# Kernel tuning notes

Measured on AMD Instinct MI355X. Metric: run time of the kernel, lower is better.

Reference implementation:

```python
import jax, jax.numpy as jnp
import numpy as np


def setup_inputs() -> dict:
    key = jax.random.key(0)
    k1, k2 = jax.random.split(key)
    x = jax.random.normal(k1, (8, 256, 16, 32, 32), dtype=jnp.float32)
    mem = jax.random.normal(k2, (200, 256), dtype=jnp.float32)
    return {"x": x, "mem": mem}


def reference(x, mem):
    B, C, T, H, W = x.shape
    # (B, N, C) tokens where N = T*H*W
    x_flat = x.reshape(B, C, -1).transpose(0, 2, 1)
    # scores against memory slots: (B, N, mem_dim)
    att = jax.nn.softmax(jnp.einsum('bnc,mc->bnm', x_flat, mem), axis=-1)
    # read from memory: (B, N, C)
    mem_out = jnp.einsum('bnm,mc->bnc', att, mem)
    return mem_out.transpose(0, 2, 1).reshape(B, C, T, H, W)
```

## Files before the change

kernel.cpp:

```cpp
#include <hip/hip_runtime.h>

typedef _Float16 h16x8 __attribute__((ext_vector_type(8)));
typedef float f32x4 __attribute__((ext_vector_type(4)));

#define MFMA16F(a, b, c) __builtin_amdgcn_mfma_f32_16x16x32_f16((a), (b), (c), 0, 0, 0)

#define GLOAD16(gp, lp)                                                        \
  __builtin_amdgcn_global_load_lds(                                            \
      (const __attribute__((address_space(1))) unsigned int*)(gp),             \
      (__attribute__((address_space(3))) unsigned int*)(lp), 16, 0, 0)

#define FENCE() __builtin_amdgcn_sched_barrier(0)


__global__ __launch_bounds__(256) void prep_mem(const float* __restrict__ mem,
                                                unsigned short* __restrict__ M16,
                                                unsigned short* __restrict__ MB) {
  const int s = blockIdx.x;
  const int c = threadIdx.x;
  const float v = (s < 200) ? mem[s * 256 + c] : 0.0f;
  const _Float16 hv = (_Float16)v;
  const unsigned short hb = __builtin_bit_cast(unsigned short, hv);
  M16[s * 256 + c] = hb;
  if (s < 224) {
    const int kk = s >> 5;
    const int th = (s >> 4) & 1;
    const int hh = (s >> 2) & 3;
    const int rr = s & 3;
    const int j = th * 4 + rr;
    MB[kk * 8192 + (c >> 4) * 512 + hh * 128 + (c & 15) * 8 + j] = hb;
  }
}

__global__ __launch_bounds__(1024, 4) void fused_mem_attn(
    const float* __restrict__ x, const unsigned short* __restrict__ M16,
    const unsigned short* __restrict__ MB, float* __restrict__ out) {
  __shared__ alignas(128) char lds[131072];

  const int tid = threadIdx.x;
  const int wave = tid >> 6;
  const int lane = tid & 63;
  const int t16 = lane & 15;
  const int h = lane >> 4;

  const int Lb = tid ^ ((tid >> 3) & 7);
  const int srcOff = (Lb >> 2) * 512 + (Lb & 3) * 16;
  const int q16 = ((((t16 << 2) + h) ^ (t16 >> 1)) << 4);

  const long gtok0 = (long)blockIdx.x * 256;
  const int b = (int)(gtok0 >> 14);
  const int bn0 = (int)(gtok0 & 16383);
  const float* xb = x + ((long)b << 22) + bn0 + (wave * 16 + t16);
  float* outT = out + ((long)b << 22) + bn0 + (wave * 16 + 4 * h) + ((long)t16 << 14);

  const char* M16B = (const char*)M16;
  const char* MBB = (const char*)MB;

#define XLOAD(ks)                                                              \
  _Pragma("unroll") for (int j = 0; j < 8; ++j) {                              \
    xr[(ks) % 3][j] = xb[(long)((ks) * 32 + h * 8 + j) << 14];                 \
  }

  float xr[3][8];
  f32x4 acc[14] = {};

#define COMPUTE(ks)                                                            \
  {                                                                            \
    if ((ks) < 6) XLOAD((ks) + 2);                                             \
    h16x8 xh, xl;                                                              \
    _Pragma("unroll") for (int j = 0; j < 8; ++j) {                            \
      const float f = xr[(ks) % 3][j];                                         \
      const _Float16 hi_ = (_Float16)f;                                        \
      xh[j] = hi_;                                                             \
      xl[j] = (_Float16)(f - (float)hi_);                                      \
    }                                                                          \
    const char* sb = lds + (ks) * 16384;                                       \
    __builtin_amdgcn_s_setprio(1);                                             \
    _Pragma("unroll") for (int tt = 0; tt < 13; ++tt) {                        \
      const h16x8 ah = *(const h16x8*)(sb + tt * 1024 + q16);                  \
      acc[tt] = MFMA16F(ah, xh, acc[tt]);                                      \
      acc[tt] = MFMA16F(ah, xl, acc[tt]);                                      \
    }                                                                          \
    __builtin_amdgcn_s_setprio(0);                                             \
    FENCE();                                                                   \
  }

  XLOAD(0);
  XLOAD(1);
#pragma unroll
  for (int ks = 0; ks < 8; ++ks)
    GLOAD16(M16B + srcOff + ks * 64, lds + ks * 16384 + tid * 16);
  __syncthreads();

  COMPUTE(0) COMPUTE(1) COMPUTE(2) COMPUTE(3)
  COMPUTE(4) COMPUTE(5) COMPUTE(6) COMPUTE(7)

  __syncthreads();

#pragma unroll
  for (int k = 0; k < 7; ++k)
    GLOAD16(MBB + k * 16384 + tid * 16, lds + k * 16384 + tid * 16);

  float m = -3.0e38f;
#pragma unroll
  for (int tt = 0; tt < 12; ++tt)
#pragma unroll
    for (int r = 0; r < 4; ++r) m = fmaxf(m, acc[tt][r]);
#pragma unroll
  for (int r = 0; r < 4; ++r)
    if (192 + h * 4 + r < 200) m = fmaxf(m, acc[12][r]);
  m = fmaxf(m, __shfl_xor(m, 16, 64));
  m = fmaxf(m, __shfl_xor(m, 32, 64));
  float s = 0.f;
#pragma unroll
  for (int tt = 0; tt < 12; ++tt)
#pragma unroll
    for (int r = 0; r < 4; ++r) {
      const float p = __expf(acc[tt][r] - m);
      acc[tt][r] = p;
      s += p;
    }
#pragma unroll
  for (int r = 0; r < 4; ++r) {
    const bool ok = (192 + h * 4 + r) < 200;
    const float p = ok ? __expf(acc[12][r] - m) : 0.f;
    acc[12][r] = p;
    s += p;
  }
  s += __shfl_xor(s, 16, 64);
  s += __shfl_xor(s, 32, 64);
  const float inv = 1.f / s;

  h16x8 pa[7];
#pragma unroll
  for (int kk = 0; kk < 7; ++kk)
#pragma unroll
    for (int j = 0; j < 8; ++j)
      pa[kk][j] = (_Float16)(inv * acc[2 * kk + (j >> 2)][j & 3]);

  __syncthreads();

#pragma unroll
  for (int ct = 0; ct < 16; ++ct) {
    f32x4 a2 = {0.f, 0.f, 0.f, 0.f};
    __builtin_amdgcn_s_setprio(1);
#pragma unroll
    for (int kk = 0; kk < 7; ++kk) {
      const h16x8 bt = *(const h16x8*)(lds + kk * 16384 + ct * 1024 + lane * 16);
      a2 = MFMA16F(pa[kk], bt, a2);
    }
    __builtin_amdgcn_s_setprio(0);
    *(f32x4*)(outT + ((long)ct << 18)) = a2;
  }
#undef XLOAD
#undef COMPUTE
}

extern "C" void kernel_launch(void* const* d_in, const int* in_sizes, int n_in,
                              void* d_out, int out_size, void* d_ws, size_t ws_size,
                              hipStream_t stream) {
  const float* x = (const float*)d_in[0];
  const float* mem = (const float*)d_in[1];
  float* out = (float*)d_out;

  unsigned short* M16 = (unsigned short*)d_ws;
  unsigned short* MB = M16 + 256 * 256;

  prep_mem<<<dim3(256), dim3(256), 0, stream>>>(mem, M16, MB);
  fused_mem_attn<<<dim3(512), dim3(1024), 0, stream>>>(x, M16, MB, out);
}
```

Baseline: 68.50 us.

## Process two token tiles per wave and shrink blocks to 768 threads

Each wave now handles 32 tokens (two 16-token groups), so every LDS-loaded memory fragment feeds two MFMAs instead of one, halving LDS reads per unit of compute. Blocks shrink to 12 waves (384 tokens) with a 342-block grid and a validity guard for the tail wave, and the shared memory staging is split across threads so all LDS slots are still filled. The setprio hints are removed, the last-slot pa fragment is zero-padded, and register pressure roughly doubles for accumulators, which risks lower occupancy or spills.

```diff
diff --git a/kernel.cpp b/kernel.cpp
--- a/kernel.cpp
+++ b/kernel.cpp
@@ -32,7 +32,7 @@
   }
 }
 
-__global__ __launch_bounds__(1024, 4) void fused_mem_attn(
+__global__ __launch_bounds__(768, 3) void fused_mem_attn(
     const float* __restrict__ x, const unsigned short* __restrict__ M16,
     const unsigned short* __restrict__ MB, float* __restrict__ out) {
   __shared__ alignas(128) char lds[131072];
@@ -43,53 +43,73 @@
   const int t16 = lane & 15;
   const int h = lane >> 4;
 
-  const int Lb = tid ^ ((tid >> 3) & 7);
-  const int srcOff = (Lb >> 2) * 512 + (Lb & 3) * 16;
+  const int P0 = tid;
+  const int L0 = P0 ^ ((P0 >> 3) & 7);
+  const int srcOff0 = (L0 >> 2) * 512 + (L0 & 3) * 16;
+  const int P1 = 768 + tid;
+  const int L1 = P1 ^ ((P1 >> 3) & 7);
+  const int srcOff1 = (L1 >> 2) * 512 + (L1 & 3) * 16;
+  const bool own1 = (tid < 256);
+
   const int q16 = ((((t16 << 2) + h) ^ (t16 >> 1)) << 4);
 
-  const long gtok0 = (long)blockIdx.x * 256;
-  const int b = (int)(gtok0 >> 14);
-  const int bn0 = (int)(gtok0 & 16383);
-  const float* xb = x + ((long)b << 22) + bn0 + (wave * 16 + t16);
-  float* outT = out + ((long)b << 22) + bn0 + (wave * 16 + 4 * h) + ((long)t16 << 14);
+  const long tw_raw = (long)blockIdx.x * 384 + wave * 32;
+  const bool wvalid = (tw_raw + 31) < 131072;
+  const long tw = wvalid ? tw_raw : 0;
+
+  const long T0 = tw + t16;
+  const long T1 = tw + 16 + t16;
+  const float* xb0 = x + ((T0 >> 14) << 22) + (T0 & 16383);
+  const float* xb1 = x + ((T1 >> 14) << 22) + (T1 & 16383);
+  const long S0 = tw + 4 * h;
+  const long S1 = tw + 16 + 4 * h;
+  float* ob0 = out + ((S0 >> 14) << 22) + (S0 & 16383) + ((long)t16 << 14);
+  float* ob1 = out + ((S1 >> 14) << 22) + (S1 & 16383) + ((long)t16 << 14);
 
   const char* M16B = (const char*)M16;
   const char* MBB = (const char*)MB;
 
 #define XLOAD(ks)                                                              \
   _Pragma("unroll") for (int j = 0; j < 8; ++j) {                              \
-    xr[(ks) % 3][j] = xb[(long)((ks) * 32 + h * 8 + j) << 14];                 \
-  }
-
-  float xr[3][8];
-  f32x4 acc[14] = {};
+    const long o_ = (long)((ks) * 32 + h * 8 + j) << 14;                       \
+    xr[(ks) & 1][0][j] = xb0[o_];                                              \
+    xr[(ks) & 1][1][j] = xb1[o_];                                              \
+  }
+
+  float xr[2][2][8];
+  f32x4 acc[13][2] = {};
 
 #define COMPUTE(ks)                                                            \
   {                                                                            \
-    if ((ks) < 6) XLOAD((ks) + 2);                                             \
-    h16x8 xh, xl;                                                              \
+    if ((ks) < 7) XLOAD((ks) + 1);                                             \
+    h16x8 xh0, xl0, xh1, xl1;                                                  \
     _Pragma("unroll") for (int j = 0; j < 8; ++j) {                            \
-      const float f = xr[(ks) % 3][j];                                         \
-      const _Float16 hi_ = (_Float16)f;                                        \
-      xh[j] = hi_;                                                             \
-      xl[j] = (_Float16)(f - (float)hi_);                                      \
+      const float f0 = xr[(ks) & 1][0][j];                                     \
+      const float f1 = xr[(ks) & 1][1][j];                                     \
+      const _Float16 h0_ = (_Float16)f0;                                       \
+      const _Float16 h1_ = (_Float16)f1;                                       \
+      xh0[j] = h0_;                                                            \
+      xl0[j] = (_Float16)(f0 - (float)h0_);                                    \
+      xh1[j] = h1_;                                                            \
+      xl1[j] = (_Float16)(f1 - (float)h1_);                                    \
     }                                                                          \
     const char* sb = lds + (ks) * 16384;                                       \
-    __builtin_amdgcn_s_setprio(1);                                             \
     _Pragma("unroll") for (int tt = 0; tt < 13; ++tt) {                        \
       const h16x8 ah = *(const h16x8*)(sb + tt * 1024 + q16);                  \
-      acc[tt] = MFMA16F(ah, xh, acc[tt]);                                      \
-      acc[tt] = MFMA16F(ah, xl, acc[tt]);                                      \
+      acc[tt][0] = MFMA16F(ah, xh0, acc[tt][0]);                               \
+      acc[tt][1] = MFMA16F(ah, xh1, acc[tt][1]);                               \
+      acc[tt][0] = MFMA16F(ah, xl0, acc[tt][0]);                               \
+      acc[tt][1] = MFMA16F(ah, xl1, acc[tt][1]);                               \
     }                                                                          \
-    __builtin_amdgcn_s_setprio(0);                                             \
     FENCE();                                                                   \
   }
 
   XLOAD(0);
-  XLOAD(1);
-#pragma unroll
-  for (int ks = 0; ks < 8; ++ks)
-    GLOAD16(M16B + srcOff + ks * 64, lds + ks * 16384 + tid * 16);
+#pragma unroll
+  for (int ks = 0; ks < 8; ++ks) {
+    GLOAD16(M16B + srcOff0 + ks * 64, lds + ks * 16384 + P0 * 16);
+    if (own1) GLOAD16(M16B + srcOff1 + ks * 64, lds + ks * 16384 + P1 * 16);
+  }
   __syncthreads();
 
   COMPUTE(0) COMPUTE(1) COMPUTE(2) COMPUTE(3)
@@ -98,59 +118,78 @@
   __syncthreads();
 
 #pragma unroll
-  for (int k = 0; k < 7; ++k)
-    GLOAD16(MBB + k * 16384 + tid * 16, lds + k * 16384 + tid * 16);
-
-  float m = -3.0e38f;
-#pragma unroll
-  for (int tt = 0; tt < 12; ++tt)
-#pragma unroll
-    for (int r = 0; r < 4; ++r) m = fmaxf(m, acc[tt][r]);
-#pragma unroll
-  for (int r = 0; r < 4; ++r)
-    if (192 + h * 4 + r < 200) m = fmaxf(m, acc[12][r]);
-  m = fmaxf(m, __shfl_xor(m, 16, 64));
-  m = fmaxf(m, __shfl_xor(m, 32, 64));
-  float s = 0.f;
-#pragma unroll
-  for (int tt = 0; tt < 12; ++tt)
+  for (int k = 0; k < 7; ++k) {
+    GLOAD16(MBB + k * 16384 + P0 * 16, lds + k * 16384 + P0 * 16);
+    if (own1) GLOAD16(MBB + k * 16384 + P1 * 16, lds + k * 16384 + P1 * 16);
+  }
+  FENCE();
+
+  float inv[2];
+#pragma unroll
+  for (int g = 0; g < 2; ++g) {
+    float m = -3.0e38f;
+#pragma unroll
+    for (int tt = 0; tt < 12; ++tt)
+#pragma unroll
+      for (int r = 0; r < 4; ++r) m = fmaxf(m, acc[tt][g][r]);
+#pragma unroll
+    for (int r = 0; r < 4; ++r)
+      if (192 + h * 4 + r < 200) m = fmaxf(m, acc[12][g][r]);
+    m = fmaxf(m, __shfl_xor(m, 16, 64));
+    m = fmaxf(m, __shfl_xor(m, 32, 64));
+    float s = 0.f;
+#pragma unroll
+    for (int tt = 0; tt < 12; ++tt)
+#pragma unroll
+      for (int r = 0; r < 4; ++r) {
+        const float p = __expf(acc[tt][g][r] - m);
+        acc[tt][g][r] = p;
+        s += p;
+      }
 #pragma unroll
     for (int r = 0; r < 4; ++r) {
-      const float p = __expf(acc[tt][r] - m);
-      acc[tt][r] = p;
+      const bool ok = (192 + h * 4 + r) < 200;
+      const float p = ok ? __expf(acc[12][g][r] - m) : 0.f;
+      acc[12][g][r] = p;
       s += p;
     }
-#pragma unroll
-  for (int r = 0; r < 4; ++r) {
-    const bool ok = (192 + h * 4 + r) < 200;
-    const float p = ok ? __expf(acc[12][r] - m) : 0.f;
-    acc[12][r] = p;
-    s += p;
-  }
-  s += __shfl_xor(s, 16, 64);
-  s += __shfl_xor(s, 32, 64);
-  const float inv = 1.f / s;
-
-  h16x8 pa[7];
-#pragma unroll
-  for (int kk = 0; kk < 7; ++kk)
+    s += __shfl_xor(s, 16, 64);
+    s += __shfl_xor(s, 32, 64);
+    inv[g] = 1.f / s;
+  }
+
+  h16x8 pa[7][2];
+#pragma unroll
+  for (int kk = 0; kk < 6; ++kk)
+#pragma unroll
+    for (int g = 0; g < 2; ++g)
+#pragma unroll
+      for (int j = 0; j < 8; ++j)
+        pa[kk][g][j] = (_Float16)(inv[g] * acc[2 * kk + (j >> 2)][g][j & 3]);
+#pragma unroll
+  for (int g = 0; g < 2; ++g)
 #pragma unroll
     for (int j = 0; j < 8; ++j)
-      pa[kk][j] = (_Float16)(inv * acc[2 * kk + (j >> 2)][j & 3]);
+      pa[6][g][j] = (j < 4) ? (_Float16)(inv[g] * acc[12][g][j & 3])
+                            : (_Float16)0.f;
 
   __syncthreads();
 
 #pragma unroll
   for (int ct = 0; ct < 16; ++ct) {
-    f32x4 a2 = {0.f, 0.f, 0.f, 0.f};
-    __builtin_amdgcn_s_setprio(1);
+    f32x4 a0 = {0.f, 0.f, 0.f, 0.f};
+    f32x4 a1 = {0.f, 0.f, 0.f, 0.f};
 #pragma unroll
     for (int kk = 0; kk < 7; ++kk) {
       const h16x8 bt = *(const h16x8*)(lds + kk * 16384 + ct * 1024 + lane * 16);
-      a2 = MFMA16F(pa[kk], bt, a2);
+      a0 = MFMA16F(pa[kk][0], bt, a0);
+      a1 = MFMA16F(pa[kk][1], bt, a1);
     }
-    __builtin_amdgcn_s_setprio(0);
-    *(f32x4*)(outT + ((long)ct << 18)) = a2;
+    if (wvalid) {
+      *(f32x4*)(ob0 + ((long)ct << 18)) = a0;
+      *(f32x4*)(ob1 + ((long)ct << 18)) = a1;
+    }
+    FENCE();
   }
 #undef XLOAD
 #undef COMPUTE
@@ -167,5 +206,5 @@
   unsigned short* MB = M16 + 256 * 256;
 
   prep_mem<<<dim3(256), dim3(256), 0, stream>>>(mem, M16, MB);
-  fused_mem_attn<<<dim3(512), dim3(1024), 0, stream>>>(x, M16, MB, out);
+  fused_mem_attn<<<dim3(342), dim3(768), 0, stream>>>(x, M16, MB, out);
 }
```

After: 84.40 us. 23.2% more time.

## Process two token tiles per block, prefetching second tile's x during first softmax

Applied to the files above, without the earlier changes.

Each block now handles 512 tokens in two sequential 256-token passes, and the grid is halved to 256 blocks. The x loads for the second tile are issued during the first tile's softmax so their latency overlaps compute. The M16 and MB tables are still re-staged into LDS for every pass, so LDS traffic is unchanged. The aim is to hide global-load latency and cut block launch overhead, at the cost of fewer blocks than the 256 CUs can use well (each block already uses 128KB of LDS) and a longer serial chain per block.

```diff
diff --git a/kernel.cpp b/kernel.cpp
--- a/kernel.cpp
+++ b/kernel.cpp
@@ -47,26 +47,35 @@
   const int srcOff = (Lb >> 2) * 512 + (Lb & 3) * 16;
   const int q16 = ((((t16 << 2) + h) ^ (t16 >> 1)) << 4);
 
-  const long gtok0 = (long)blockIdx.x * 256;
-  const int b = (int)(gtok0 >> 14);
-  const int bn0 = (int)(gtok0 & 16383);
-  const float* xb = x + ((long)b << 22) + bn0 + (wave * 16 + t16);
-  float* outT = out + ((long)b << 22) + bn0 + (wave * 16 + 4 * h) + ((long)t16 << 14);
+  const long base0 = (long)blockIdx.x * 512;
+  const int b = (int)(base0 >> 14);
+  const int bn0 = (int)(base0 & 16383);
+  const float* xA = x + ((long)b << 22) + bn0 + (wave * 16 + t16);
+  const float* xBp = xA + 256;
+  float* oA = out + ((long)b << 22) + bn0 + (wave * 16 + 4 * h) + ((long)t16 << 14);
+  float* oB = oA + 256;
 
   const char* M16B = (const char*)M16;
   const char* MBB = (const char*)MB;
 
-#define XLOAD(ks)                                                              \
+  float xr[3][8];
+
+#define STAGE_M16()                                                            \
+  _Pragma("unroll") for (int ks = 0; ks < 8; ++ks)                             \
+      GLOAD16(M16B + srcOff + ks * 64, lds + ks * 16384 + tid * 16);
+
+#define STAGE_MB()                                                             \
+  _Pragma("unroll") for (int k = 0; k < 7; ++k)                                \
+      GLOAD16(MBB + k * 16384 + tid * 16, lds + k * 16384 + tid * 16);
+
+#define XLOAD(XP, ks)                                                          \
   _Pragma("unroll") for (int j = 0; j < 8; ++j) {                              \
-    xr[(ks) % 3][j] = xb[(long)((ks) * 32 + h * 8 + j) << 14];                 \
-  }
-
-  float xr[3][8];
-  f32x4 acc[14] = {};
-
-#define COMPUTE(ks)                                                            \
+    xr[(ks) % 3][j] = (XP)[(long)((ks) * 32 + h * 8 + j) << 14];               \
+  }
+
+#define COMPUTE(XP, ks)                                                        \
   {                                                                            \
-    if ((ks) < 6) XLOAD((ks) + 2);                                             \
+    if ((ks) < 6) XLOAD(XP, (ks) + 2);                                         \
     h16x8 xh, xl;                                                              \
     _Pragma("unroll") for (int j = 0; j < 8; ++j) {                            \
       const float f = xr[(ks) % 3][j];                                         \
@@ -85,75 +94,101 @@
     FENCE();                                                                   \
   }
 
-  XLOAD(0);
-  XLOAD(1);
-#pragma unroll
-  for (int ks = 0; ks < 8; ++ks)
-    GLOAD16(M16B + srcOff + ks * 64, lds + ks * 16384 + tid * 16);
+#define SOFTMAX_REPACK()                                                       \
+  {                                                                            \
+    float m = -3.0e38f;                                                        \
+    _Pragma("unroll") for (int tt = 0; tt < 12; ++tt)                          \
+        _Pragma("unroll") for (int r = 0; r < 4; ++r)                          \
+            m = fmaxf(m, acc[tt][r]);                                          \
+    _Pragma("unroll") for (int r = 0; r < 4; ++r)                              \
+        if (192 + h * 4 + r < 200) m = fmaxf(m, acc[12][r]);                   \
+    m = fmaxf(m, __shfl_xor(m, 16, 64));                                       \
+    m = fmaxf(m, __shfl_xor(m, 32, 64));                                       \
+    float s = 0.f;                                                             \
+    _Pragma("unroll") for (int tt = 0; tt < 12; ++tt)                          \
+        _Pragma("unroll") for (int r = 0; r < 4; ++r) {                        \
+      const float p = __expf(acc[tt][r] - m);                                  \
+      acc[tt][r] = p;                                                          \
+      s += p;                                                                  \
+    }                                                                          \
+    _Pragma("unroll") for (int r = 0; r < 4; ++r) {                            \
+      const bool ok = (192 + h * 4 + r) < 200;                                 \
+      const float p = ok ? __expf(acc[12][r] - m) : 0.f;                       \
+      acc[12][r] = p;                                                          \
+      s += p;                                                                  \
+    }                                                                          \
+    s += __shfl_xor(s, 16, 64);                                                \
+    s += __shfl_xor(s, 32, 64);                                                \
+    const float inv = 1.f / s;                                                 \
+    _Pragma("unroll") for (int kk = 0; kk < 7; ++kk)                           \
+        _Pragma("unroll") for (int j = 0; j < 8; ++j)                          \
+            pa[kk][j] = (_Float16)(inv * acc[2 * kk + (j >> 2)][j & 3]);       \
+  }
+
+#define PV_PHASE(OB)                                                           \
+  _Pragma("unroll") for (int ct = 0; ct < 16; ++ct) {                          \
+    f32x4 a2 = {0.f, 0.f, 0.f, 0.f};                                           \
+    __builtin_amdgcn_s_setprio(1);                                             \
+    _Pragma("unroll") for (int kk = 0; kk < 7; ++kk) {                         \
+      const h16x8 bt =                                                         \
+          *(const h16x8*)(lds + kk * 16384 + ct * 1024 + lane * 16);           \
+      a2 = MFMA16F(pa[kk], bt, a2);                                            \
+    }                                                                          \
+    __builtin_amdgcn_s_setprio(0);                                             \
+    *(f32x4*)((OB) + ((long)ct << 18)) = a2;                                   \
+  }
+
+  {
+    XLOAD(xA, 0);
+    XLOAD(xA, 1);
+    STAGE_M16();
+    __syncthreads();
+
+    f32x4 acc[14] = {};
+    h16x8 pa[7];
+
+    COMPUTE(xA, 0) COMPUTE(xA, 1) COMPUTE(xA, 2) COMPUTE(xA, 3)
+    COMPUTE(xA, 4) COMPUTE(xA, 5) COMPUTE(xA, 6) COMPUTE(xA, 7)
+
+    __syncthreads();
+    STAGE_MB();
+    XLOAD(xBp, 0);
+    XLOAD(xBp, 1);
+
+    SOFTMAX_REPACK();
+
+    __syncthreads();
+
+    PV_PHASE(oA);
+  }
+
   __syncthreads();
 
-  COMPUTE(0) COMPUTE(1) COMPUTE(2) COMPUTE(3)
-  COMPUTE(4) COMPUTE(5) COMPUTE(6) COMPUTE(7)
-
-  __syncthreads();
-
-#pragma unroll
-  for (int k = 0; k < 7; ++k)
-    GLOAD16(MBB + k * 16384 + tid * 16, lds + k * 16384 + tid * 16);
-
-  float m = -3.0e38f;
-#pragma unroll
-  for (int tt = 0; tt < 12; ++tt)
-#pragma unroll
-    for (int r = 0; r < 4; ++r) m = fmaxf(m, acc[tt][r]);
-#pragma unroll
-  for (int r = 0; r < 4; ++r)
-    if (192 + h * 4 + r < 200) m = fmaxf(m, acc[12][r]);
-  m = fmaxf(m, __shfl_xor(m, 16, 64));
-  m = fmaxf(m, __shfl_xor(m, 32, 64));
-  float s = 0.f;
-#pragma unroll
-  for (int tt = 0; tt < 12; ++tt)
-#pragma unroll
-    for (int r = 0; r < 4; ++r) {
-      const float p = __expf(acc[tt][r] - m);
-      acc[tt][r] = p;
-      s += p;
-    }
-#pragma unroll
-  for (int r = 0; r < 4; ++r) {
-    const bool ok = (192 + h * 4 + r) < 200;
-    const float p = ok ? __expf(acc[12][r] - m) : 0.f;
-    acc[12][r] = p;
-    s += p;
-  }
-  s += __shfl_xor(s, 16, 64);
-  s += __shfl_xor(s, 32, 64);
-  const float inv = 1.f / s;
-
-  h16x8 pa[7];
-#pragma unroll
-  for (int kk = 0; kk < 7; ++kk)
-#pragma unroll
-    for (int j = 0; j < 8; ++j)
-      pa[kk][j] = (_Float16)(inv * acc[2 * kk + (j >> 2)][j & 3]);
-
-  __syncthreads();
-
-#pragma unroll
-  for (int ct = 0; ct < 16; ++ct) {
-    f32x4 a2 = {0.f, 0.f, 0.f, 0.f};
-    __builtin_amdgcn_s_setprio(1);
-#pragma unroll
-    for (int kk = 0; kk < 7; ++kk) {
-      const h16x8 bt = *(const h16x8*)(lds + kk * 16384 + ct * 1024 + lane * 16);
-      a2 = MFMA16F(pa[kk], bt, a2);
-    }
-    __builtin_amdgcn_s_setprio(0);
-    *(f32x4*)(outT + ((long)ct << 18)) = a2;
-  }
+  {
+    STAGE_M16();
+    __syncthreads();
+
+    f32x4 acc[14] = {};
+    h16x8 pa[7];
+
+    COMPUTE(xBp, 0) COMPUTE(xBp, 1) COMPUTE(xBp, 2) COMPUTE(xBp, 3)
+    COMPUTE(xBp, 4) COMPUTE(xBp, 5) COMPUTE(xBp, 6) COMPUTE(xBp, 7)
+
+    __syncthreads();
+    STAGE_MB();
+
+    SOFTMAX_REPACK();
+
+    __syncthreads();
+
+    PV_PHASE(oB);
+  }
+#undef STAGE_M16
+#undef STAGE_MB
 #undef XLOAD
 #undef COMPUTE
+#undef SOFTMAX_REPACK
+#undef PV_PHASE
 }
 
 extern "C" void kernel_launch(void* const* d_in, const int* in_sizes, int n_in,
@@ -167,5 +202,5 @@
   unsigned short* MB = M16 + 256 * 256;
 
   prep_mem<<<dim3(256), dim3(256), 0, stream>>>(mem, M16, MB);
-  fused_mem_attn<<<dim3(512), dim3(1024), 0, stream>>>(x, M16, MB, out);
+  fused_mem_attn<<<dim3(256), dim3(1024), 0, stream>>>(x, M16, MB, out);
 }
```

New measurement: 143.0 us. 109% more time.
